# Kernel optimization log

Measured on AMD Instinct MI355X. Metric: run time of the kernel, lower is better.

The kernel has to match this reference:

```python
import jax, jax.numpy as jnp
import numpy as np

V, C, T, H, HS, HID, L = 8000, 256, 256, 4, 64, 1024, 2
B = 2


def _ln(x, g, b, eps=1e-5):
    mu = jnp.mean(x, axis=-1, keepdims=True)
    var = jnp.var(x, axis=-1, keepdims=True)
    return (x - mu) * jax.lax.rsqrt(var + eps) * g + b


def setup_inputs() -> dict:
    key = jax.random.key(0)
    ks = iter(jax.random.split(key, 32))
    n = lambda shape: jax.random.normal(next(ks), shape, dtype=jnp.float32) * 0.02
    inp = {
        "idx": jax.random.randint(next(ks), (B, T), 0, V),
        "tok_emb": n((V, C)),
        # distance positional embedding params
        "pos_table": n((T, C)),
        "pos_w1": n((C, 2 * C)),
        "pos_w2": n((2 * C, 2 * C)),
        "pos_b2": n((2 * C,)),
        "pos_ln_g": jnp.ones((2 * C,), jnp.float32),
        "pos_ln_b": jnp.zeros((2 * C,), jnp.float32),
        # per-layer, per-head attention-MLP params (stacked over L, H)
        "att_w1": n((L, H, 2 * C, C)),
        "att_w2": n((L, H, C)),
        "att_b2": n((L, H)),
        "val_w": n((L, H, C, HS)),
        "proj_w": n((L, C, C)),
        "proj_b": n((L, C)),
        "ln2_g": jnp.ones((L, C), jnp.float32),
        "ln2_b": jnp.zeros((L, C), jnp.float32),
        "ff_w1": n((L, C, HID)),
        "ff_w2": n((L, HID, C)),
        "ff_b2": n((L, C)),
        "lnf_g": jnp.ones((C,), jnp.float32),
        "lnf_b": jnp.zeros((C,), jnp.float32),
        "head_w": n((C, V)),
        "head_b": n((V,)),
    }
    return inp


def reference(idx, tok_emb, pos_table, pos_w1, pos_w2, pos_b2, pos_ln_g, pos_ln_b,
              att_w1, att_w2, att_b2, val_w, proj_w, proj_b, ln2_g, ln2_b,
              ff_w1, ff_w2, ff_b2, lnf_g, lnf_b, head_w, head_b):
    b, t = idx.shape
    gelu = lambda x: jax.nn.gelu(x, approximate=False)

    # distance positional embedding: tril(i - j) indices into table
    ar = jnp.arange(t)
    dist = jnp.tril(ar[:, None] - ar[None, :])            # [t,t] in [0, t)
    pe = pos_table[dist]                                   # [t,t,C]
    pe = gelu(pe @ pos_w1) @ pos_w2 + pos_b2               # [t,t,2C]
    pe = _ln(pe, pos_ln_g, pos_ln_b)                       # [t,t,2C]

    mask = jnp.tril(jnp.ones((t, t), bool))                # causal
    scale = C ** (-0.5)

    x = tok_emb[idx]                                       # [b,t,C]
    for l in range(L):
        # pairwise concat(key, query) + pos emb, shared across heads
        kk = jnp.broadcast_to(x[:, None, :, :], (b, t, t, C))   # k[b,i,j]=x[b,j]
        qq = jnp.broadcast_to(x[:, :, None, :], (b, t, t, C))   # q[b,i,j]=x[b,i]
        a2 = jnp.concatenate([kk, qq], axis=-1) + pe[None]       # [b,t,t,2C]
        h1 = gelu(jnp.einsum('btsz,hzc->bhtsc', a2, att_w1[l]))  # [b,H,t,t,C]
        wei = jnp.einsum('bhtsc,hc->bhts', h1, att_w2[l]) + att_b2[l][None, :, None, None]
        wei = wei * scale
        wei = jnp.where(mask[None, None], wei, -jnp.inf)
        wei = jax.nn.softmax(wei, axis=-1)                       # [b,H,t,t]
        v = jnp.einsum('btc,hcd->bhtd', x, val_w[l])             # [b,H,t,HS]
        out = jnp.einsum('bhts,bhsd->bhtd', wei, v)              # [b,H,t,HS]
        out = out.transpose(0, 2, 1, 3).reshape(b, t, H * HS)    # concat heads
        x = x + out @ proj_w[l] + proj_b[l]
        h = _ln(x, ln2_g[l], ln2_b[l])
        x = x + gelu(h @ ff_w1[l]) @ ff_w2[l] + ff_b2[l]
    x = _ln(x, lnf_g, lnf_b)
    logits = x @ head_w + head_b                                 # [b,t,V]
    return logits
```

## Files before the change

kernel.cpp:

```cpp
#include <hip/hip_runtime.h>
#include <hip/hip_bf16.h>
#include <math.h>

constexpr int TDIM = 256;
constexpr int CDIM = 256;
constexpr int NH   = 4;
constexpr int DHS  = 64;
constexpr int FHID = 1024;
constexpr int NV   = 8000;
constexpr int NB   = 2;

typedef __attribute__((ext_vector_type(8))) short bf16x8;
typedef __attribute__((ext_vector_type(4))) float f32x4;
typedef __attribute__((ext_vector_type(2))) float f32x2;
typedef __attribute__((ext_vector_type(4))) unsigned int uint4v;

__device__ __forceinline__ float gelu_f(float x) {
    return 0.5f * x * (1.0f + erff(x * 0.70710678118654752440f));
}

__device__ __forceinline__ f32x2 gelu2(f32x2 x) {
    constexpr float kA = 2.0f * 1.4426950408889634f * 0.7978845608028654f;
    constexpr float kB = kA * 0.044715f;
    f32x2 arg = x * (kA + kB * (x * x));
    arg.x = fminf(arg.x, 120.f);
    arg.y = fminf(arg.y, 120.f);
    float e0 = exp2f(arg.x), e1 = exp2f(arg.y);
    f32x2 num; num.x = x.x * e0; num.y = x.y * e1;
    f32x2 den; den.x = __builtin_amdgcn_rcpf(e0 + 1.f); den.y = __builtin_amdgcn_rcpf(e1 + 1.f);
    return num * den;
}

__device__ __forceinline__ unsigned short f2bf(float f) {
    unsigned int u = __float_as_uint(f);
    unsigned int r = (u + 0x7FFF + ((u >> 16) & 1)) >> 16;
    return (unsigned short)r;
}

__global__ __launch_bounds__(256) void k_tcast_all(
    const float* __restrict__ head_w, const float* __restrict__ att_w1,
    const float* __restrict__ ff_w1, const float* __restrict__ ff_w2,
    const float* __restrict__ val_w, const float* __restrict__ proj_w,
    unsigned short* __restrict__ wT, unsigned short* __restrict__ W1r,
    unsigned short* __restrict__ Wff1, unsigned short* __restrict__ Wff2,
    unsigned short* __restrict__ Wv, unsigned short* __restrict__ Wproj)
{
    int q = blockIdx.x;
    const float* src; unsigned short* dst; int R, C, tx, ty;
    if (q < 2000)      { src = head_w; dst = wT; R = 256; C = 8000; tx = q % 250; ty = q / 250; }
    else if (q < 3024) { int u = q - 2000, s = u >> 7, v = u & 127;
        src = att_w1 + (size_t)s * 512 * 256; dst = W1r + (size_t)s * 512 * 256;
        R = 512; C = 256; tx = v & 7; ty = v >> 3; }
    else if (q < 3536) { int u = q - 3024, s = u >> 8, v = u & 255;
        src = ff_w1 + (size_t)s * 256 * 1024; dst = Wff1 + (size_t)s * 256 * 1024;
        R = 256; C = 1024; tx = v & 31; ty = v >> 5; }
    else if (q < 4048) { int u = q - 3536, s = u >> 8, v = u & 255;
        src = ff_w2 + (size_t)s * 1024 * 256; dst = Wff2 + (size_t)s * 1024 * 256;
        R = 1024; C = 256; tx = v & 7; ty = v >> 3; }
    else if (q < 4176) { int u = q - 4048, s = u >> 4, v = u & 15;
        src = val_w + (size_t)s * 256 * 64; dst = Wv + (size_t)s * 256 * 64;
        R = 256; C = 64; tx = v & 1; ty = v >> 1; }
    else { int u = q - 4176, s = u >> 6, v = u & 63;
        src = proj_w + (size_t)s * 256 * 256; dst = Wproj + (size_t)s * 256 * 256;
        R = 256; C = 256; tx = v & 7; ty = v >> 3; }
    __shared__ float tile[32][33];
    int c0 = tx * 32, r0 = ty * 32, t = threadIdx.x;
    #pragma unroll
    for (int e = 0; e < 4; ++e) {
        int lin = e * 256 + t; int rr = lin >> 5, cc = lin & 31;
        tile[rr][cc] = src[(size_t)(r0 + rr) * C + c0 + cc];
    }
    __syncthreads();
    #pragma unroll
    for (int e = 0; e < 4; ++e) {
        int lin = e * 256 + t; int cc = lin >> 5, rr = lin & 31;
        dst[(size_t)(c0 + cc) * R + r0 + rr] = f2bf(tile[rr][cc]);
    }
}

__global__ __launch_bounds__(512) void k_pre(
    const int* __restrict__ idx, const float* __restrict__ tok_emb,
    const float* __restrict__ pos_table, const float* __restrict__ pos_w1,
    const float* __restrict__ pos_w2, const float* __restrict__ pos_b2,
    const float* __restrict__ g, const float* __restrict__ bb,
    float* __restrict__ x, unsigned short* __restrict__ x_bf,
    unsigned short* __restrict__ ped_bf)
{
    int bid = blockIdx.x;
    int t = threadIdx.x;
    if (bid < 256) {
        int r = bid * 2 + (t >> 8);
        int c = t & 255;
        int tok = idx[r];
        float v = tok_emb[(size_t)tok * CDIM + c];
        x[r * CDIM + c] = v;
        x_bf[r * CDIM + c] = f2bf(v);
        return;
    }
    int d = bid - 256;
    __shared__ float xs[CDIM];
    __shared__ float hs[512];
    __shared__ float red[512];
    if (t < CDIM) xs[t] = pos_table[d * CDIM + t];
    __syncthreads();
    float acc = 0.f;
    for (int c = 0; c < CDIM; ++c) acc += xs[c] * pos_w1[(size_t)c * 512 + t];
    hs[t] = gelu_f(acc);
    __syncthreads();
    float acc2 = pos_b2[t];
    for (int z = 0; z < 512; ++z) acc2 += hs[z] * pos_w2[(size_t)z * 512 + t];
    red[t] = acc2; __syncthreads();
    for (int s = 256; s > 0; s >>= 1) { if (t < s) red[t] += red[t + s]; __syncthreads(); }
    float mean = red[0] * (1.f / 512.f); __syncthreads();
    float dv = acc2 - mean;
    red[t] = dv * dv; __syncthreads();
    for (int s = 256; s > 0; s >>= 1) { if (t < s) red[t] += red[t + s]; __syncthreads(); }
    float r = rsqrtf(red[0] * (1.f / 512.f) + 1e-5f);
    ped_bf[d * 512 + t] = f2bf(dv * r * g[t] + bb[t]);
}

__device__ __forceinline__ void gemm64_core(
    const unsigned short* __restrict__ A, int lda,
    const unsigned short* __restrict__ B, int ldb,
    int kLen, int t, f32x4 acc[2][2],
    unsigned short* __restrict__ A_lds, unsigned short* __restrict__ B_lds)
{
    int lane = t & 63;
    int w = t >> 6;
    int wm = (w >> 1) * 32, wn = (w & 1) * 32;
    int l15 = lane & 15;
    int lk = (lane >> 4) * 8;
    for (int kc = 0; kc < kLen; kc += 128) {
        #pragma unroll
        for (int it = 0; it < 4; ++it) {
            int chunk = it * 256 + t;
            int row = chunk >> 4;
            int c16 = chunk & 15;
            uint4v va = *(const uint4v*)(A + (size_t)row * lda + kc + c16 * 8);
            uint4v vb = *(const uint4v*)(B + (size_t)row * ldb + kc + c16 * 8);
            int lin = row * 256 + c16 * 16;
            int phys = lin ^ ((row & 7) << 4);
            *(uint4v*)((char*)A_lds + phys) = va;
            *(uint4v*)((char*)B_lds + phys) = vb;
        }
        __syncthreads();
        #pragma unroll
        for (int ks = 0; ks < 4; ++ks) {
            int kb = ks * 32 + lk;
            bf16x8 a[2], b[2];
            #pragma unroll
            for (int f = 0; f < 2; ++f) {
                int mrow = wm + f * 16 + l15;
                int lina = mrow * 256 + kb * 2;
                a[f] = *(const bf16x8*)((const char*)A_lds + (lina ^ ((mrow & 7) << 4)));
                int nrow = wn + f * 16 + l15;
                int linb = nrow * 256 + kb * 2;
                b[f] = *(const bf16x8*)((const char*)B_lds + (linb ^ ((nrow & 7) << 4)));
            }
            acc[0][0] = __builtin_amdgcn_mfma_f32_16x16x32_bf16(a[0], b[0], acc[0][0], 0, 0, 0);
            acc[0][1] = __builtin_amdgcn_mfma_f32_16x16x32_bf16(a[0], b[1], acc[0][1], 0, 0, 0);
            acc[1][0] = __builtin_amdgcn_mfma_f32_16x16x32_bf16(a[1], b[0], acc[1][0], 0, 0, 0);
            acc[1][1] = __builtin_amdgcn_mfma_f32_16x16x32_bf16(a[1], b[1], acc[1][1], 0, 0, 0);
        }
        __syncthreads();
    }
}

__global__ __launch_bounds__(256) void k_qkv(
    const unsigned short* __restrict__ x_bf,
    const unsigned short* __restrict__ ped_bf,
    const unsigned short* __restrict__ W1r,
    const unsigned short* __restrict__ Wv,
    float* __restrict__ PT, float* __restrict__ Qb, float* __restrict__ RT,
    float* __restrict__ vbuf, int l)
{
    __shared__ unsigned short A_lds[64 * 128];
    __shared__ unsigned short B_lds[64 * 128];
    int t = threadIdx.x;
    int bid = blockIdx.x;
    int lane = t & 63, w = t >> 6;
    int wm = (w >> 1) * 32, wn = (w & 1) * 32;
    int l15 = lane & 15;
    f32x4 acc[2][2] = {};
    if (bid < 256) {
        int r0 = (bid & 7) * 64;
        int n0 = (bid >> 3) * 64;
        int h = n0 >> 9, isQ = (n0 >> 8) & 1;
        const unsigned short* Bp = W1r + (size_t)l * 1024 * 512
                                 + (size_t)(h * 256 + (n0 & 255)) * 512 + isQ * 256;
        gemm64_core(x_bf + (size_t)r0 * 256, 256, Bp, 512, 256, t, acc, A_lds, B_lds);
        #pragma unroll
        for (int fm = 0; fm < 2; ++fm)
        #pragma unroll
        for (int fn = 0; fn < 2; ++fn) {
            int col = n0 + wn + fn * 16 + l15;
            int c = col & 255;
            #pragma unroll
            for (int r = 0; r < 4; ++r) {
                int row = r0 + wm + fm * 16 + (lane >> 4) * 4 + r;
                int b = row >> 8, ij = row & 255;
                if (isQ) Qb[((b * TDIM + ij) * NH + h) * CDIM + c] = acc[fm][fn][r];
                else     PT[((size_t)(b * NH + h) * CDIM + c) * TDIM + ij] = acc[fm][fn][r];
            }
        }
    } else if (bid < 320) {
        int u = bid - 256;
        int r0 = (u & 3) * 64;
        int n0 = (u >> 2) * 64;
        const unsigned short* Bp = W1r + (size_t)l * 1024 * 512 + (size_t)n0 * 512;
        gemm64_core(ped_bf + (size_t)r0 * 512, 512, Bp, 512, 512, t, acc, A_lds, B_lds);
        #pragma unroll
        for (int fm = 0; fm < 2; ++fm)
        #pragma unroll
        for (int fn = 0; fn < 2; ++fn) {
            int col = n0 + wn + fn * 16 + l15;
            #pragma unroll
            for (int r = 0; r < 4; ++r) {
                int d = r0 + wm + fm * 16 + (lane >> 4) * 4 + r;
                RT[(size_t)col * TDIM + d] = acc[fm][fn][r];
            }
        }
    } else {
        int u = bid - 320;
        int r0 = (u & 7) * 64;
        int n0 = (u >> 3) * 64;
        int h = n0 >> 6;
        const unsigned short* Bp = Wv + ((size_t)l * NH + h) * DHS * CDIM;
        gemm64_core(x_bf + (size_t)r0 * 256, 256, Bp, 256, 256, t, acc, A_lds, B_lds);
        #pragma unroll
        for (int fm = 0; fm < 2; ++fm)
        #pragma unroll
        for (int fn = 0; fn < 2; ++fn) {
            int col = n0 + wn + fn * 16 + l15;
            int d = col & 63;
            #pragma unroll
            for (int r = 0; r < 4; ++r) {
                int row = r0 + wm + fm * 16 + (lane >> 4) * 4 + r;
                int b = row >> 8, j = row & 255;
                vbuf[((size_t)(b * NH + h) * TDIM + j) * DHS + d] = acc[fm][fn][r];
            }
        }
    }
}

__global__ __launch_bounds__(1024, 8) void k_wei(
    const float* __restrict__ PT, const float* __restrict__ Qb,
    const float* __restrict__ RT, const float* __restrict__ att_w2,
    const float* __restrict__ att_b2, const float* __restrict__ vbuf,
    int l, unsigned short* __restrict__ attn_bf) {
    int bid = blockIdx.x;
    int bh = bid & 7;
    int b = bh >> 2, h = bh & 3;
    int i0 = (63 - (bid >> 3)) * 4;
    int t = threadIdx.x;
    int j = t & 255;
    int cs = t >> 8;
    __shared__ float shQW[256][8];
    __shared__ float part[4][4][256];
    __shared__ float p_lds[4][256];
    __shared__ float pvp[4][4][64];
    { int ii = t >> 8, c = t & 255;
      shQW[c][ii] = Qb[((b * TDIM + (i0 + ii)) * NH + h) * CDIM + c]; }
    if (t < 256) shQW[t][4] = att_w2[(l * NH + h) * CDIM + t];
    __syncthreads();
    f32x2 accA = {0.f, 0.f}, accB = {0.f, 0.f};
    int m = i0 - j;
    int mm = max(m, -3);
    if ((t & 192) <= i0 + 3) {
        const float* pk = PT + ((size_t)(b * NH + h) * CDIM + cs * 64) * TDIM + j;
        const float* rk = RT + ((size_t)h * CDIM + cs * 64) * TDIM + mm;
        float p_n = *pk;
        f32x4 r_n; __builtin_memcpy(&r_n, rk, 16);
        #pragma unroll 4
        for (int k = 0; k < 64; ++k) {
            float p_c = p_n; f32x4 r_c = r_n;
            pk += TDIM; rk += TDIM;
            if (k < 63) { p_n = *pk; __builtin_memcpy(&r_n, rk, 16); }
            int c = cs * 64 + k;
            f32x4 q4 = *(const f32x4*)(&shQW[c][0]);
            float w2v = shQW[c][4];
            f32x2 zA, zB;
            zA.x = p_c + q4.x + r_c.x; zA.y = p_c + q4.y + r_c.y;
            zB.x = p_c + q4.z + r_c.z; zB.y = p_c + q4.w + r_c.w;
            accA += gelu2(zA) * w2v;
            accB += gelu2(zB) * w2v;
        }
    }
    part[cs][0][j] = accA.x; part[cs][1][j] = accA.y;
    part[cs][2][j] = accB.x; part[cs][3][j] = accB.y;
    __syncthreads();
    if (t < 256) {
        #pragma unroll
        for (int ii = 0; ii < 4; ++ii) {
            float s = part[0][ii][t] + part[1][ii][t] + part[2][ii][t] + part[3][ii][t];
            part[0][ii][t] = s;
        }
    }
    __syncthreads();
    if (t < 256) {
        float b2 = att_b2[l * NH + h];
        int lane = t & 63, w = t >> 6;
        int i = i0 + w;
        float lv[4];
        #pragma unroll
        for (int s = 0; s < 4; ++s) {
            int jj = lane + s * 64;
            lv[s] = (jj <= i) ? (part[0][w][jj] + b2) * 0.0625f : -1e30f;
        }
        float mx = fmaxf(fmaxf(lv[0], lv[1]), fmaxf(lv[2], lv[3]));
        #pragma unroll
        for (int off = 32; off; off >>= 1) mx = fmaxf(mx, __shfl_xor(mx, off));
        float es[4], sum = 0.f;
        #pragma unroll
        for (int s = 0; s < 4; ++s) { es[s] = exp2f((lv[s] - mx) * 1.4426950409f); sum += es[s]; }
        #pragma unroll
        for (int off = 32; off; off >>= 1) sum += __shfl_xor(sum, off);
        float inv = 1.0f / sum;
        #pragma unroll
        for (int s = 0; s < 4; ++s) p_lds[w][lane + s * 64] = es[s] * inv;
    }
    __syncthreads();
    {
        int strip = t >> 8, row = (t >> 6) & 3, d = t & 63;
        const float* vp = vbuf + ((size_t)(b * NH + h) * TDIM + strip * 64) * DHS + d;
        const float* pl = &p_lds[row][strip * 64];
        float acc = 0.f;
        #pragma unroll 8
        for (int jj = 0; jj < 64; ++jj)
            acc = fmaf(pl[jj], vp[(size_t)jj * DHS], acc);
        pvp[strip][row][d] = acc;
    }
    __syncthreads();
    if (t < 256) {
        int row = t >> 6, d = t & 63;
        float s = pvp[0][row][d] + pvp[1][row][d] + pvp[2][row][d] + pvp[3][row][d];
        attn_bf[((size_t)(b * TDIM + i0 + row)) * CDIM + h * DHS + d] = f2bf(s);
    }
}

__global__ __launch_bounds__(256) void k_proj_gemm(
    const unsigned short* __restrict__ attn_bf,
    const unsigned short* __restrict__ Wproj,
    const float* __restrict__ proj_b,
    float* __restrict__ pbuf, int l)
{
    __shared__ unsigned short A_lds[64 * 128];
    __shared__ unsigned short B_lds[64 * 128];
    int t = threadIdx.x;
    int r0 = (blockIdx.x & 7) * 64;
    int n0 = (blockIdx.x >> 3) * 64;
    f32x4 acc[2][2] = {};
    gemm64_core(attn_bf + (size_t)r0 * 256, 256,
                Wproj + (size_t)l * 65536 + (size_t)n0 * 256, 256, 256, t, acc, A_lds, B_lds);
    int lane = t & 63, w = t >> 6;
    int wm = (w >> 1) * 32, wn = (w & 1) * 32;
    int l15 = lane & 15;
    #pragma unroll
    for (int fm = 0; fm < 2; ++fm)
    #pragma unroll
    for (int fn = 0; fn < 2; ++fn) {
        int col = n0 + wn + fn * 16 + l15;
        float bb = proj_b[l * CDIM + col];
        #pragma unroll
        for (int r = 0; r < 4; ++r) {
            int row = r0 + wm + fm * 16 + (lane >> 4) * 4 + r;
            pbuf[(size_t)row * CDIM + col] = acc[fm][fn][r] + bb;
        }
    }
}

__global__ void k_resln(const float* __restrict__ pbuf, float* __restrict__ x,
                        const float* __restrict__ lg, const float* __restrict__ lb,
                        unsigned short* __restrict__ hbuf_bf) {
    int bi = blockIdx.x;
    int t = threadIdx.x;
    __shared__ float red[CDIM];
    float val = x[bi * CDIM + t] + pbuf[bi * CDIM + t];
    x[bi * CDIM + t] = val;
    red[t] = val; __syncthreads();
    for (int s = 128; s > 0; s >>= 1) { if (t < s) red[t] += red[t + s]; __syncthreads(); }
    float mean = red[0] * (1.f / 256.f); __syncthreads();
    float dv = val - mean;
    red[t] = dv * dv; __syncthreads();
    for (int s = 128; s > 0; s >>= 1) { if (t < s) red[t] += red[t + s]; __syncthreads(); }
    float r = rsqrtf(red[0] * (1.f / 256.f) + 1e-5f);
    hbuf_bf[bi * CDIM + t] = f2bf(dv * r * lg[t] + lb[t]);
}

__global__ __launch_bounds__(256) void k_ff1_gemm(
    const unsigned short* __restrict__ hbuf_bf,
    const unsigned short* __restrict__ Wff1,
    unsigned short* __restrict__ fbuf_bf, int l)
{
    __shared__ unsigned short A_lds[64 * 128];
    __shared__ unsigned short B_lds[64 * 128];
    int t = threadIdx.x;
    int r0 = blockIdx.x * 64;
    int n0 = blockIdx.y * 64;
    const unsigned short* Bp = Wff1 + (size_t)l * 1024 * 256 + (size_t)n0 * 256;
    f32x4 acc[2][2] = {};
    gemm64_core(hbuf_bf + (size_t)r0 * 256, 256, Bp, 256, 256, t, acc, A_lds, B_lds);
    int lane = t & 63, w = t >> 6;
    int wm = (w >> 1) * 32, wn = (w & 1) * 32;
    int l15 = lane & 15;
    #pragma unroll
    for (int fm = 0; fm < 2; ++fm)
    #pragma unroll
    for (int fn = 0; fn < 2; ++fn) {
        int col = n0 + wn + fn * 16 + l15;
        #pragma unroll
        for (int r = 0; r < 4; ++r) {
            int row = r0 + wm + fm * 16 + (lane >> 4) * 4 + r;
            fbuf_bf[(size_t)row * FHID + col] = f2bf(gelu_f(acc[fm][fn][r]));
        }
    }
}

__global__ __launch_bounds__(256) void k_ff2_gemm(
    const unsigned short* __restrict__ fbuf_bf,
    const unsigned short* __restrict__ Wff2,
    const float* __restrict__ ff_b2,
    float* __restrict__ x, unsigned short* __restrict__ x_bf, int l)
{
    __shared__ unsigned short A_lds[64 * 128];
    __shared__ unsigned short B_lds[64 * 128];
    int t = threadIdx.x;
    int r0 = blockIdx.x * 64;
    int n0 = blockIdx.y * 64;
    const unsigned short* Bp = Wff2 + (size_t)l * 256 * 1024 + (size_t)n0 * 1024;
    f32x4 acc[2][2] = {};
    gemm64_core(fbuf_bf + (size_t)r0 * 1024, 1024, Bp, 1024, 1024, t, acc, A_lds, B_lds);
    int lane = t & 63, w = t >> 6;
    int wm = (w >> 1) * 32, wn = (w & 1) * 32;
    int l15 = lane & 15;
    #pragma unroll
    for (int fm = 0; fm < 2; ++fm)
    #pragma unroll
    for (int fn = 0; fn < 2; ++fn) {
        int col = n0 + wn + fn * 16 + l15;
        float bb = ff_b2[l * CDIM + col];
        #pragma unroll
        for (int r = 0; r < 4; ++r) {
            int row = r0 + wm + fm * 16 + (lane >> 4) * 4 + r;
            float v = x[(size_t)row * CDIM + col] + acc[fm][fn][r] + bb;
            x[(size_t)row * CDIM + col] = v;
            x_bf[(size_t)row * CDIM + col] = f2bf(v);
        }
    }
}

__global__ void k_lnf_bf16(const float* __restrict__ x, const float* __restrict__ g,
                           const float* __restrict__ bb, unsigned short* __restrict__ out) {
    int bi = blockIdx.x;
    int t = threadIdx.x;
    __shared__ float red[CDIM];
    float val = x[bi * CDIM + t];
    red[t] = val; __syncthreads();
    for (int s = 128; s > 0; s >>= 1) { if (t < s) red[t] += red[t + s]; __syncthreads(); }
    float mean = red[0] * (1.f / 256.f); __syncthreads();
    float dv = val - mean;
    red[t] = dv * dv; __syncthreads();
    for (int s = 128; s > 0; s >>= 1) { if (t < s) red[t] += red[t + s]; __syncthreads(); }
    float r = rsqrtf(red[0] * (1.f / 256.f) + 1e-5f);
    out[bi * CDIM + t] = f2bf(dv * r * g[t] + bb[t]);
}

__global__ __launch_bounds__(256) void k_head_mfma(
    const unsigned short* __restrict__ xf_bf,
    const unsigned short* __restrict__ wT,
    const float* __restrict__ head_b,
    float* __restrict__ out)
{
    __shared__ unsigned short A_lds[64 * 128];
    __shared__ unsigned short B_lds[64 * 128];
    int t = threadIdx.x;
    int r0 = blockIdx.x * 64;
    int n0 = blockIdx.y * 64;
    f32x4 acc[2][2] = {};
    gemm64_core(xf_bf + (size_t)r0 * 256, 256, wT + (size_t)n0 * 256, 256, 256,
                t, acc, A_lds, B_lds);
    int lane = t & 63, w = t >> 6;
    int wm = (w >> 1) * 32, wn = (w & 1) * 32;
    int l15 = lane & 15;
    #pragma unroll
    for (int fm = 0; fm < 2; ++fm)
    #pragma unroll
    for (int fn = 0; fn < 2; ++fn) {
        int col = n0 + wn + fn * 16 + l15;
        float hb = head_b[col];
        #pragma unroll
        for (int r = 0; r < 4; ++r) {
            int row = r0 + wm + fm * 16 + (lane >> 4) * 4 + r;
            out[(size_t)row * NV + col] = acc[fm][fn][r] + hb;
        }
    }
}

extern "C" void kernel_launch(void* const* d_in, const int* in_sizes, int n_in,
                              void* d_out, int out_size, void* d_ws, size_t ws_size,
                              hipStream_t stream) {
    const int*   idx       = (const int*)  d_in[0];
    const float* tok_emb   = (const float*)d_in[1];
    const float* pos_table = (const float*)d_in[2];
    const float* pos_w1    = (const float*)d_in[3];
    const float* pos_w2    = (const float*)d_in[4];
    const float* pos_b2    = (const float*)d_in[5];
    const float* pos_ln_g  = (const float*)d_in[6];
    const float* pos_ln_b  = (const float*)d_in[7];
    const float* att_w1    = (const float*)d_in[8];
    const float* att_w2    = (const float*)d_in[9];
    const float* att_b2    = (const float*)d_in[10];
    const float* val_w     = (const float*)d_in[11];
    const float* proj_w    = (const float*)d_in[12];
    const float* proj_b    = (const float*)d_in[13];
    const float* ln2_g     = (const float*)d_in[14];
    const float* ln2_b     = (const float*)d_in[15];
    const float* ff_w1     = (const float*)d_in[16];
    const float* ff_w2     = (const float*)d_in[17];
    const float* ff_b2     = (const float*)d_in[18];
    const float* lnf_g     = (const float*)d_in[19];
    const float* lnf_b     = (const float*)d_in[20];
    const float* head_w    = (const float*)d_in[21];
    const float* head_b    = (const float*)d_in[22];
    float* out = (float*)d_out;

    float* ws = (float*)d_ws;
    float* x    = ws;  ws += NB * TDIM * CDIM;
    float* PT   = ws;  ws += NB * NH * CDIM * TDIM;
    float* Qb   = ws;  ws += NB * TDIM * NH * CDIM;
    ws += 16;
    float* RT   = ws;  ws += NH * CDIM * TDIM;
    float* vbuf = ws;  ws += NB * NH * TDIM * DHS;
    float* pbuf = PT;
    unsigned short* x_bf    = (unsigned short*)ws; ws += NB * TDIM * CDIM / 2;
    unsigned short* ped_bf  = (unsigned short*)ws; ws += TDIM * 2 * CDIM / 2;
    unsigned short* hbuf_bf = (unsigned short*)ws; ws += NB * TDIM * CDIM / 2;
    unsigned short* xf_bf   = (unsigned short*)ws; ws += NB * TDIM * CDIM / 2;
    unsigned short* attn_bf = (unsigned short*)ws; ws += NB * TDIM * CDIM / 2;
    unsigned short* fbuf_bf = (unsigned short*)ws; ws += NB * TDIM * FHID / 2;
    unsigned short* wT      = (unsigned short*)ws; ws += NV * CDIM / 2;
    unsigned short* W1r     = (unsigned short*)ws; ws += 2 * 1024 * 512 / 2;
    unsigned short* Wff1    = (unsigned short*)ws; ws += 2 * 1024 * 256 / 2;
    unsigned short* Wff2    = (unsigned short*)ws; ws += 2 * 256 * 1024 / 2;
    unsigned short* Wv      = (unsigned short*)ws; ws += 2 * NH * DHS * CDIM / 2;
    unsigned short* Wproj   = (unsigned short*)ws; ws += 2 * CDIM * CDIM / 2;

    k_tcast_all<<<4304, 256, 0, stream>>>(head_w, att_w1, ff_w1, ff_w2, val_w, proj_w,
                                          wT, W1r, Wff1, Wff2, Wv, Wproj);
    k_pre<<<512, 512, 0, stream>>>(idx, tok_emb, pos_table, pos_w1, pos_w2, pos_b2,
                                   pos_ln_g, pos_ln_b, x, x_bf, ped_bf);

    for (int l = 0; l < 2; ++l) {
        k_qkv<<<352, 256, 0, stream>>>(x_bf, ped_bf, W1r, Wv, PT, Qb, RT, vbuf, l);
        k_wei<<<NB * NH * TDIM / 4, 1024, 0, stream>>>(PT, Qb, RT, att_w2, att_b2, vbuf,
                                                       l, attn_bf);
        k_proj_gemm<<<32, 256, 0, stream>>>(attn_bf, Wproj, proj_b, pbuf, l);
        k_resln<<<NB * TDIM, 256, 0, stream>>>(pbuf, x, ln2_g + l * CDIM, ln2_b + l * CDIM, hbuf_bf);
        k_ff1_gemm<<<dim3(8, 16), 256, 0, stream>>>(hbuf_bf, Wff1, fbuf_bf, l);
        k_ff2_gemm<<<dim3(8, 4), 256, 0, stream>>>(fbuf_bf, Wff2, ff_b2, x, x_bf, l);
    }

    k_lnf_bf16<<<NB * TDIM, 256, 0, stream>>>(x, lnf_g, lnf_b, xf_bf);
    k_head_mfma<<<dim3(8, 125), 256, 0, stream>>>(xf_bf, wT, head_b, out);
}
```

Baseline: 352.4 us.

## Split attention-value product into separate MFMA GEMM and rebalance wei work across waves

The weight kernel now only computes attention scores and softmax, writing bf16 probabilities to a workspace buffer. A new MFMA GEMM kernel multiplies them by a bf16 transposed value matrix that the qkv kernel now emits. Inside the score kernel, the causal range is split adaptively across 1, 2 or 4 key strips with finer channel chunks, so waves no longer idle on masked-out keys. This adds a kernel launch and a round trip of the probability matrix through global memory, and bf16 probabilities and values cost some precision.

```diff
diff --git a/kernel.cpp b/kernel.cpp
--- a/kernel.cpp
+++ b/kernel.cpp
@@ -172,7 +172,7 @@
     const unsigned short* __restrict__ W1r,
     const unsigned short* __restrict__ Wv,
     float* __restrict__ PT, float* __restrict__ Qb, float* __restrict__ RT,
-    float* __restrict__ vbuf, int l)
+    unsigned short* __restrict__ vT_bf, int l)
 {
     __shared__ unsigned short A_lds[64 * 128];
     __shared__ unsigned short B_lds[64 * 128];
@@ -237,7 +237,7 @@
             for (int r = 0; r < 4; ++r) {
                 int row = r0 + wm + fm * 16 + (lane >> 4) * 4 + r;
                 int b = row >> 8, j = row & 255;
-                vbuf[((size_t)(b * NH + h) * TDIM + j) * DHS + d] = acc[fm][fn][r];
+                vT_bf[(((size_t)b * NH + h) * DHS + d) * TDIM + j] = f2bf(acc[fm][fn][r]);
             }
         }
     }
@@ -246,66 +246,70 @@
 __global__ __launch_bounds__(1024, 8) void k_wei(
     const float* __restrict__ PT, const float* __restrict__ Qb,
     const float* __restrict__ RT, const float* __restrict__ att_w2,
-    const float* __restrict__ att_b2, const float* __restrict__ vbuf,
-    int l, unsigned short* __restrict__ attn_bf) {
+    const float* __restrict__ att_b2, int l, unsigned short* __restrict__ wei_bf) {
     int bid = blockIdx.x;
     int bh = bid & 7;
     int b = bh >> 2, h = bh & 3;
     int i0 = (63 - (bid >> 3)) * 4;
     int t = threadIdx.x;
-    int j = t & 255;
-    int cs = t >> 8;
+    int wid = t >> 6, lane = t & 63;
+    int nlog = (i0 + 4 <= 64) ? 0 : (i0 + 4 <= 128) ? 1 : 2;
+    int ns = 1 << nlog;
+    int nchunks = 16 >> nlog;
+    int c_len = 16 << nlog;
+    int strip = wid & (ns - 1);
+    int cchunk = wid >> nlog;
+    int c0 = cchunk * c_len;
+    int j = strip * 64 + lane;
     __shared__ float shQW[256][8];
-    __shared__ float part[4][4][256];
-    __shared__ float p_lds[4][256];
-    __shared__ float pvp[4][4][64];
+    __shared__ float part[16][4][64];
     { int ii = t >> 8, c = t & 255;
       shQW[c][ii] = Qb[((b * TDIM + (i0 + ii)) * NH + h) * CDIM + c]; }
     if (t < 256) shQW[t][4] = att_w2[(l * NH + h) * CDIM + t];
     __syncthreads();
     f32x2 accA = {0.f, 0.f}, accB = {0.f, 0.f};
-    int m = i0 - j;
-    int mm = max(m, -3);
-    if ((t & 192) <= i0 + 3) {
-        const float* pk = PT + ((size_t)(b * NH + h) * CDIM + cs * 64) * TDIM + j;
-        const float* rk = RT + ((size_t)h * CDIM + cs * 64) * TDIM + mm;
-        float p_n = *pk;
-        f32x4 r_n; __builtin_memcpy(&r_n, rk, 16);
+    int mm = max(i0 - j, -3);
+    {
+        const float* pk = PT + ((size_t)(b * NH + h) * CDIM + c0) * TDIM + j;
+        const float* rk = RT + ((size_t)h * CDIM + c0) * TDIM + mm;
         #pragma unroll 4
-        for (int k = 0; k < 64; ++k) {
-            float p_c = p_n; f32x4 r_c = r_n;
+        for (int k = 0; k < c_len; ++k) {
+            float p = *pk;
+            f32x4 r4; __builtin_memcpy(&r4, rk, 16);
             pk += TDIM; rk += TDIM;
-            if (k < 63) { p_n = *pk; __builtin_memcpy(&r_n, rk, 16); }
-            int c = cs * 64 + k;
+            int c = c0 + k;
             f32x4 q4 = *(const f32x4*)(&shQW[c][0]);
             float w2v = shQW[c][4];
             f32x2 zA, zB;
-            zA.x = p_c + q4.x + r_c.x; zA.y = p_c + q4.y + r_c.y;
-            zB.x = p_c + q4.z + r_c.z; zB.y = p_c + q4.w + r_c.w;
+            zA.x = p + q4.x + r4.x; zA.y = p + q4.y + r4.y;
+            zB.x = p + q4.z + r4.z; zB.y = p + q4.w + r4.w;
             accA += gelu2(zA) * w2v;
             accB += gelu2(zB) * w2v;
         }
     }
-    part[cs][0][j] = accA.x; part[cs][1][j] = accA.y;
-    part[cs][2][j] = accB.x; part[cs][3][j] = accB.y;
+    part[wid][0][lane] = accA.x; part[wid][1][lane] = accA.y;
+    part[wid][2][lane] = accB.x; part[wid][3][lane] = accB.y;
     __syncthreads();
     if (t < 256) {
-        #pragma unroll
-        for (int ii = 0; ii < 4; ++ii) {
-            float s = part[0][ii][t] + part[1][ii][t] + part[2][ii][t] + part[3][ii][t];
-            part[0][ii][t] = s;
-        }
+        int jj = t, sj = jj >> 6, l6 = jj & 63;
+        float s0 = 0, s1 = 0, s2 = 0, s3 = 0;
+        for (int cc = 0; cc < nchunks; ++cc) {
+            int w = ((cc << nlog) + sj) & 15;
+            s0 += part[w][0][l6]; s1 += part[w][1][l6];
+            s2 += part[w][2][l6]; s3 += part[w][3][l6];
+        }
+        shQW[jj][0] = s0; shQW[jj][1] = s1; shQW[jj][2] = s2; shQW[jj][3] = s3;
     }
     __syncthreads();
     if (t < 256) {
         float b2 = att_b2[l * NH + h];
-        int lane = t & 63, w = t >> 6;
+        int l6 = t & 63, w = t >> 6;
         int i = i0 + w;
         float lv[4];
         #pragma unroll
         for (int s = 0; s < 4; ++s) {
-            int jj = lane + s * 64;
-            lv[s] = (jj <= i) ? (part[0][w][jj] + b2) * 0.0625f : -1e30f;
+            int jj = l6 + s * 64;
+            lv[s] = (jj <= i) ? (shQW[jj][w] + b2) * 0.0625f : -1e30f;
         }
         float mx = fmaxf(fmaxf(lv[0], lv[1]), fmaxf(lv[2], lv[3]));
         #pragma unroll
@@ -316,25 +320,40 @@
         #pragma unroll
         for (int off = 32; off; off >>= 1) sum += __shfl_xor(sum, off);
         float inv = 1.0f / sum;
-        #pragma unroll
-        for (int s = 0; s < 4; ++s) p_lds[w][lane + s * 64] = es[s] * inv;
-    }
-    __syncthreads();
-    {
-        int strip = t >> 8, row = (t >> 6) & 3, d = t & 63;
-        const float* vp = vbuf + ((size_t)(b * NH + h) * TDIM + strip * 64) * DHS + d;
-        const float* pl = &p_lds[row][strip * 64];
-        float acc = 0.f;
-        #pragma unroll 8
-        for (int jj = 0; jj < 64; ++jj)
-            acc = fmaf(pl[jj], vp[(size_t)jj * DHS], acc);
-        pvp[strip][row][d] = acc;
-    }
-    __syncthreads();
-    if (t < 256) {
-        int row = t >> 6, d = t & 63;
-        float s = pvp[0][row][d] + pvp[1][row][d] + pvp[2][row][d] + pvp[3][row][d];
-        attn_bf[((size_t)(b * TDIM + i0 + row)) * CDIM + h * DHS + d] = f2bf(s);
+        unsigned short* wrow = wei_bf + (((size_t)bh * TDIM) + i) * TDIM;
+        #pragma unroll
+        for (int s = 0; s < 4; ++s) wrow[l6 + s * 64] = f2bf(es[s] * inv);
+    }
+}
+
+__global__ __launch_bounds__(256) void k_av_gemm(
+    const unsigned short* __restrict__ wei_bf,
+    const unsigned short* __restrict__ vT_bf,
+    unsigned short* __restrict__ attn_bf)
+{
+    __shared__ unsigned short A_lds[64 * 128];
+    __shared__ unsigned short B_lds[64 * 128];
+    int t = threadIdx.x;
+    int bid = blockIdx.x;
+    int bh = bid >> 2;
+    int r0 = (bid & 3) * 64;
+    int b = bh >> 2, h = bh & 3;
+    f32x4 acc[2][2] = {};
+    gemm64_core(wei_bf + (size_t)bh * 65536 + (size_t)r0 * 256, 256,
+                vT_bf + (size_t)bh * 16384, 256, 256, t, acc, A_lds, B_lds);
+    int lane = t & 63, w = t >> 6;
+    int wm = (w >> 1) * 32, wn = (w & 1) * 32;
+    int l15 = lane & 15;
+    #pragma unroll
+    for (int fm = 0; fm < 2; ++fm)
+    #pragma unroll
+    for (int fn = 0; fn < 2; ++fn) {
+        int d = wn + fn * 16 + l15;
+        #pragma unroll
+        for (int r = 0; r < 4; ++r) {
+            int i = r0 + wm + fm * 16 + (lane >> 4) * 4 + r;
+            attn_bf[((size_t)(b * TDIM + i)) * CDIM + h * DHS + d] = f2bf(acc[fm][fn][r]);
+        }
     }
 }
 
@@ -530,20 +549,21 @@
     float* Qb   = ws;  ws += NB * TDIM * NH * CDIM;
     ws += 16;
     float* RT   = ws;  ws += NH * CDIM * TDIM;
-    float* vbuf = ws;  ws += NB * NH * TDIM * DHS;
     float* pbuf = PT;
     unsigned short* x_bf    = (unsigned short*)ws; ws += NB * TDIM * CDIM / 2;
     unsigned short* ped_bf  = (unsigned short*)ws; ws += TDIM * 2 * CDIM / 2;
     unsigned short* hbuf_bf = (unsigned short*)ws; ws += NB * TDIM * CDIM / 2;
     unsigned short* xf_bf   = (unsigned short*)ws; ws += NB * TDIM * CDIM / 2;
+    unsigned short* wei_bf  = (unsigned short*)ws; ws += NB * NH * TDIM * TDIM / 2;
+    unsigned short* vT_bf   = (unsigned short*)ws; ws += NB * NH * DHS * TDIM / 2;
     unsigned short* attn_bf = (unsigned short*)ws; ws += NB * TDIM * CDIM / 2;
-    unsigned short* fbuf_bf = (unsigned short*)ws; ws += NB * TDIM * FHID / 2;
     unsigned short* wT      = (unsigned short*)ws; ws += NV * CDIM / 2;
     unsigned short* W1r     = (unsigned short*)ws; ws += 2 * 1024 * 512 / 2;
     unsigned short* Wff1    = (unsigned short*)ws; ws += 2 * 1024 * 256 / 2;
     unsigned short* Wff2    = (unsigned short*)ws; ws += 2 * 256 * 1024 / 2;
     unsigned short* Wv      = (unsigned short*)ws; ws += 2 * NH * DHS * CDIM / 2;
     unsigned short* Wproj   = (unsigned short*)ws; ws += 2 * CDIM * CDIM / 2;
+    unsigned short* fbuf_bf = wei_bf;
 
     k_tcast_all<<<4304, 256, 0, stream>>>(head_w, att_w1, ff_w1, ff_w2, val_w, proj_w,
                                           wT, W1r, Wff1, Wff2, Wv, Wproj);
@@ -551,9 +571,9 @@
                                    pos_ln_g, pos_ln_b, x, x_bf, ped_bf);
 
     for (int l = 0; l < 2; ++l) {
-        k_qkv<<<352, 256, 0, stream>>>(x_bf, ped_bf, W1r, Wv, PT, Qb, RT, vbuf, l);
-        k_wei<<<NB * NH * TDIM / 4, 1024, 0, stream>>>(PT, Qb, RT, att_w2, att_b2, vbuf,
-                                                       l, attn_bf);
+        k_qkv<<<352, 256, 0, stream>>>(x_bf, ped_bf, W1r, Wv, PT, Qb, RT, vT_bf, l);
+        k_wei<<<NB * NH * TDIM / 4, 1024, 0, stream>>>(PT, Qb, RT, att_w2, att_b2, l, wei_bf);
+        k_av_gemm<<<32, 256, 0, stream>>>(wei_bf, vT_bf, attn_bf);
         k_proj_gemm<<<32, 256, 0, stream>>>(attn_bf, Wproj, proj_b, pbuf, l);
         k_resln<<<NB * TDIM, 256, 0, stream>>>(pbuf, x, ln2_g + l * CDIM, ln2_b + l * CDIM, hbuf_bf);
         k_ff1_gemm<<<dim3(8, 16), 256, 0, stream>>>(hbuf_bf, Wff1, fbuf_bf, l);
```

Result: faster. 320.4 us (-9.1%).
